# Optimization experiments

Measured on AMD Instinct MI355X. Metric: run time of the kernel, lower is better.

Reference implementation:

```python
import jax, jax.numpy as jnp
import numpy as np

# ControllerLayer hyperparams (match init_kwargs)
ALPHA = 0.01
TOP_K = 2
TEMPERATURE = 1.0  # temperature == 1.0 -> no division (use_temperature False)


def setup_inputs() -> dict:
    key = jax.random.key(0)
    k1, k2 = jax.random.split(key)
    B, H, C, D = 8, 32, 2048, 128  # batch, n_heads(=output_dim), seq_len, head_dim(=input_dim)
    x = jax.random.normal(k1, (B, H, C, D), dtype=jnp.float32)
    # router projection weight, torch nn.Linear(input_dim, output_dim, bias=False) -> W: (output_dim, input_dim)
    W = jax.random.normal(k2, (H, D), dtype=jnp.float32) * (1.0 / np.sqrt(D).astype(np.float32))
    return {"x": x, "W": W}


def reference(x, W):
    # x: (B, H, C, D) -- q reshaped per-head features; W: (O, D) with O == H
    B, H, C, D = x.shape
    O = W.shape[0]
    logits = jnp.einsum('bhcd,od->bhco', x, W)          # router logits
    probs = jax.nn.softmax(logits, axis=-1)             # (B, H, C, O)
    topk_probs, topk_idx = jax.lax.top_k(probs, TOP_K)  # (B, H, C, K)

    # torch.gather along dim=1 (head axis): sel[b,h,c,j,d] = x[b, topk_idx[b,h,c,j], c, d]
    xb = jnp.broadcast_to(x[:, :, :, None, :], (B, H, C, TOP_K, D))
    idx = jnp.broadcast_to(topk_idx[..., None], (B, H, C, TOP_K, D))
    sel = jnp.take_along_axis(xb, idx, axis=1)          # (B, H, C, K, D)

    # weighted sum over the k selected heads
    y = jnp.einsum('bhck,bhckd->bhcd', topk_probs, sel)

    # auxiliary load-balancing loss
    router_probs = probs.mean(axis=(0, 1, 2))                                   # (O,)
    counts = jnp.zeros((O,), jnp.float32).at[topk_idx.ravel()].add(1.0)         # bincount
    router_fraction = counts / counts.sum()
    aux_loss = ALPHA * O * jnp.sum(router_probs * router_fraction)
    return y, aux_loss
```

## Files before the change

kernel.cpp:

```cpp
#include <hip/hip_runtime.h>

#define NSLOT 256

typedef double dbl4 __attribute__((ext_vector_type(4)));
typedef float  f32x4 __attribute__((ext_vector_type(4)));

__global__ __launch_bounds__(256) void convert_w_kernel(const float* __restrict__ W,
                                                        double* __restrict__ wd) {
  int i = blockIdx.x * 256 + threadIdx.x;
  int d4 = i >> 7;
  int o  = (i >> 2) & 31;
  int k  = i & 3;
  wd[i] = (double)W[(o << 7) + (d4 << 2) + k];
}

__global__ __launch_bounds__(256, 4) void moe_router_kernel(
    const float* __restrict__ x, const double* __restrict__ wd,
    float* __restrict__ y, float* __restrict__ ws) {
  __shared__ float  Xs[64 * 128];
  __shared__ double m1s[4][64];
  __shared__ double m2s[4][64];
  __shared__ int    jps[4][64];
  __shared__ float  sumS[4][64];

  const int tid = threadIdx.x;
  const int l   = tid & 63;
  const int wu  = __builtin_amdgcn_readfirstlane(tid >> 6);
  const int bc  = blockIdx.x;
  const int b   = bc >> 10;
  const int c0  = (bc & 1023) << 1;

  const float* xb = x + ((size_t)b * 32 * 2048 + c0) * 128;

  {
    auto ldsX = (__attribute__((address_space(3))) char*)Xs;
    #pragma unroll
    for (int rep = 0; rep < 8; ++rep) {
      int i   = (rep << 8) + tid;
      int row = i >> 5;
      int p   = i & 31;
      int h   = row & 31, t = row >> 5;
      int d4  = p ^ (row & 31);
      const float* src = xb + ((size_t)h * 2048 + t) * 128 + (d4 << 2);
      __builtin_amdgcn_global_load_lds(
          (const __attribute__((address_space(1))) void*)src,
          (__attribute__((address_space(3))) void*)(ldsX + (size_t)i * 16),
          16, 0, 0);
    }
  }
  __syncthreads();

  double acc[8] = {0, 0, 0, 0, 0, 0, 0, 0};
  const dbl4* __restrict__ wv4 = reinterpret_cast<const dbl4*>(wd);
  const int rsw = l & 31;
  #pragma unroll 2
  for (int d4 = 0; d4 < 32; ++d4) {
    float4 xv = *reinterpret_cast<const float4*>(&Xs[(l << 7) + ((d4 ^ rsw) << 2)]);
    double x0 = (double)xv.x, x1 = (double)xv.y, x2 = (double)xv.z, x3 = (double)xv.w;
    const dbl4* wc = wv4 + (d4 << 5) + (wu << 3);
    #pragma unroll
    for (int j = 0; j < 8; ++j) {
      dbl4 wj = wc[j];
      acc[j] = fma(x0, wj[0], acc[j]);
      acc[j] = fma(x1, wj[1], acc[j]);
      acc[j] = fma(x2, wj[2], acc[j]);
      acc[j] = fma(x3, wj[3], acc[j]);
    }
  }

  double m1 = acc[0], m2 = -1.0e300;
  int    j1 = 0, j2 = 0;
  #pragma unroll
  for (int j = 1; j < 8; ++j) {
    double v = acc[j];
    if (v > m1)      { m2 = m1; j2 = j1; m1 = v; j1 = j; }
    else if (v > m2) { m2 = v; j2 = j; }
  }
  float e[8];
  float sloc = 0.0f;
  #pragma unroll
  for (int j = 0; j < 8; ++j) { e[j] = __expf((float)(acc[j] - m1)); sloc += e[j]; }

  m1s[wu][l]  = m1;
  m2s[wu][l]  = m2;
  jps[wu][l]  = (j1 + (wu << 3)) | ((j2 + (wu << 3)) << 8);
  sumS[wu][l] = sloc;
  __syncthreads();

  double M = -1.0e300, g2 = -1.0e300;
  int g1i = 0, g2i = 0;
  #pragma unroll
  for (int w = 0; w < 4; ++w) {
    double a  = m1s[w][l];
    double bb = m2s[w][l];
    int    jp = jps[w][l];
    if (a > M)       { g2 = M; g2i = g1i; M = a; g1i = jp & 255; }
    else if (a > g2) { g2 = a; g2i = jp & 255; }
    if (bb > g2)     { g2 = bb; g2i = (jp >> 8) & 255; }
  }
  float S = 0.0f;
  #pragma unroll
  for (int w = 0; w < 4; ++w)
    S += sumS[w][l] * __expf((float)(m1s[w][l] - M));
  const float invS = 1.0f / S;
  const float p1 = invS;
  const float p2 = __expf((float)(g2 - M)) * invS;
  const int   jpack = g1i | (g2i << 8);

  {
    const float f = __expf((float)(m1 - M)) * invS;
    float ps[8];
    #pragma unroll
    for (int j = 0; j < 8; ++j) ps[j] = e[j] * f;
    #pragma unroll
    for (int m = 1; m < 64; m <<= 1) {
      #pragma unroll
      for (int j = 0; j < 8; ++j) ps[j] += __shfl_xor(ps[j], m, 64);
    }
    const int slot = (bc & (NSLOT - 1)) << 5;
    if (l == 0) {
      #pragma unroll
      for (int j = 0; j < 8; ++j) atomicAdd(&ws[slot + (wu << 3) + j], ps[j]);
    }
    if (wu == 0) {
      float cnt = 0.0f;
      #pragma unroll
      for (int o = 0; o < 32; ++o) {
        float c = (float)(__popcll(__ballot(g1i == o)) + __popcll(__ballot(g2i == o)));
        if (l == o) cnt = c;
      }
      if (l < 32) atomicAdd(&ws[8192 + slot + l], cnt);
    }
  }

  float* yb = y + ((size_t)b * 32 * 2048 + c0) * 128;
  #pragma unroll
  for (int rep = 0; rep < 8; ++rep) {
    int i   = (rep << 8) + tid;
    int row = i >> 5;
    int d4  = i & 31;
    float q1 = __shfl(p1, row, 64);
    float q2 = __shfl(p2, row, 64);
    int   jp = __shfl(jpack, row, 64);
    int i1 = jp & 255, i2 = (jp >> 8) & 255;
    int t = row >> 5, h = row & 31;
    const float4 A  = *reinterpret_cast<const float4*>(
        &Xs[(((t << 5) + i1) << 7) + ((d4 ^ i1) << 2)]);
    const float4 Bv = *reinterpret_cast<const float4*>(
        &Xs[(((t << 5) + i2) << 7) + ((d4 ^ i2) << 2)]);
    f32x4 o4;
    o4.x = q1 * A.x + q2 * Bv.x;
    o4.y = q1 * A.y + q2 * Bv.y;
    o4.z = q1 * A.z + q2 * Bv.z;
    o4.w = q1 * A.w + q2 * Bv.w;
    __builtin_nontemporal_store(o4,
        reinterpret_cast<f32x4*>(yb + ((size_t)h * 2048 + t) * 128 + (d4 << 2)));
  }
}

__global__ __launch_bounds__(256) void finalize_kernel(const float* __restrict__ ws,
                                                       float* __restrict__ out_aux) {
  __shared__ double redP[8][32];
  __shared__ double redC[8][32];
  const int o = threadIdx.x & 31;
  const int g = threadIdx.x >> 5;
  double sp = 0.0, sc = 0.0;
  for (int s = g; s < NSLOT; s += 8) {
    sp += (double)ws[s * 32 + o];
    sc += (double)ws[8192 + s * 32 + o];
  }
  redP[g][o] = sp;
  redC[g][o] = sc;
  __syncthreads();
  if (threadIdx.x == 0) {
    double aux = 0.0;
    const double nrows  = 524288.0;
    const double ntotal = 1048576.0;
    for (int oo = 0; oo < 32; ++oo) {
      double tp = 0.0, tc = 0.0;
      for (int gg = 0; gg < 8; ++gg) { tp += redP[gg][oo]; tc += redC[gg][oo]; }
      aux += (tp / nrows) * (tc / ntotal);
    }
    out_aux[0] = (float)(0.01 * 32.0 * aux);
  }
}

extern "C" void kernel_launch(void* const* d_in, const int* in_sizes, int n_in,
                              void* d_out, int out_size, void* d_ws, size_t ws_size,
                              hipStream_t stream) {
  const float* x = (const float*)d_in[0];
  const float* W = (const float*)d_in[1];
  float*  y  = (float*)d_out;
  float*  ws = (float*)d_ws;
  double* wd = (double*)((char*)d_ws + 65536);

  (void)hipMemsetAsync(d_ws, 0, 16384 * sizeof(float), stream);
  convert_w_kernel<<<16, 256, 0, stream>>>(W, wd);
  moe_router_kernel<<<8192, 256, 0, stream>>>(x, wd, y, ws);
  finalize_kernel<<<1, 256, 0, stream>>>(ws, y + (size_t)8 * 32 * 2048 * 128);
}
```

Before: 194.0 us.

## Use 512-thread blocks splitting experts across 8 waves and fold memset into prep

The router block grows from 4 to 8 wavefronts, so each wave computes logits for 4 experts instead of 8. This halves per-thread FP64 accumulators and adds an LDS prefetch of the next x chunk inside the dot-product loop. The separate hipMemsetAsync is merged into the W-conversion kernel to cut one launch. The cost is a larger cross-wave reduction, more LDS for the per-wave partials, and a different occupancy trade-off.

```diff
diff --git a/kernel.cpp b/kernel.cpp
--- a/kernel.cpp
+++ b/kernel.cpp
@@ -5,23 +5,27 @@
 typedef double dbl4 __attribute__((ext_vector_type(4)));
 typedef float  f32x4 __attribute__((ext_vector_type(4)));
 
-__global__ __launch_bounds__(256) void convert_w_kernel(const float* __restrict__ W,
-                                                        double* __restrict__ wd) {
+__global__ __launch_bounds__(256) void prep_kernel(const float* __restrict__ W,
+                                                   double* __restrict__ wd,
+                                                   float* __restrict__ ws) {
   int i = blockIdx.x * 256 + threadIdx.x;
-  int d4 = i >> 7;
-  int o  = (i >> 2) & 31;
-  int k  = i & 3;
-  wd[i] = (double)W[(o << 7) + (d4 << 2) + k];
-}
-
-__global__ __launch_bounds__(256, 4) void moe_router_kernel(
+  ws[i] = 0.0f;
+  if (i < 4096) {
+    int d4 = i >> 7;
+    int o  = (i >> 2) & 31;
+    int k  = i & 3;
+    wd[i] = (double)W[(o << 7) + (d4 << 2) + k];
+  }
+}
+
+__global__ __launch_bounds__(512, 6) void moe_router_kernel(
     const float* __restrict__ x, const double* __restrict__ wd,
     float* __restrict__ y, float* __restrict__ ws) {
   __shared__ float  Xs[64 * 128];
-  __shared__ double m1s[4][64];
-  __shared__ double m2s[4][64];
-  __shared__ int    jps[4][64];
-  __shared__ float  sumS[4][64];
+  __shared__ double m1s[8][64];
+  __shared__ double m2s[8][64];
+  __shared__ int    jps[8][64];
+  __shared__ float  sumS[8][64];
 
   const int tid = threadIdx.x;
   const int l   = tid & 63;
@@ -35,8 +39,8 @@
   {
     auto ldsX = (__attribute__((address_space(3))) char*)Xs;
     #pragma unroll
-    for (int rep = 0; rep < 8; ++rep) {
-      int i   = (rep << 8) + tid;
+    for (int rep = 0; rep < 4; ++rep) {
+      int i   = (rep << 9) + tid;
       int row = i >> 5;
       int p   = i & 31;
       int h   = row & 31, t = row >> 5;
@@ -50,47 +54,53 @@
   }
   __syncthreads();
 
-  double acc[8] = {0, 0, 0, 0, 0, 0, 0, 0};
+  double a0 = 0.0, a1 = 0.0, a2 = 0.0, a3 = 0.0;
   const dbl4* __restrict__ wv4 = reinterpret_cast<const dbl4*>(wd);
-  const int rsw = l & 31;
-  #pragma unroll 2
+  const int rsw  = l & 31;
+  const int base = l << 7;
+  float4 xv = *reinterpret_cast<const float4*>(&Xs[base + (rsw << 2)]);
+  #pragma unroll 4
   for (int d4 = 0; d4 < 32; ++d4) {
-    float4 xv = *reinterpret_cast<const float4*>(&Xs[(l << 7) + ((d4 ^ rsw) << 2)]);
+    float4 xn = *reinterpret_cast<const float4*>(
+        &Xs[base + ((((d4 + 1) & 31) ^ rsw) << 2)]);
+    const dbl4* wc = wv4 + (d4 << 5) + (wu << 2);
+    dbl4 w0 = wc[0], w1 = wc[1], w2 = wc[2], w3 = wc[3];
     double x0 = (double)xv.x, x1 = (double)xv.y, x2 = (double)xv.z, x3 = (double)xv.w;
-    const dbl4* wc = wv4 + (d4 << 5) + (wu << 3);
-    #pragma unroll
-    for (int j = 0; j < 8; ++j) {
-      dbl4 wj = wc[j];
-      acc[j] = fma(x0, wj[0], acc[j]);
-      acc[j] = fma(x1, wj[1], acc[j]);
-      acc[j] = fma(x2, wj[2], acc[j]);
-      acc[j] = fma(x3, wj[3], acc[j]);
-    }
-  }
-
+    a0 = fma(x0, w0[0], a0); a0 = fma(x1, w0[1], a0);
+    a0 = fma(x2, w0[2], a0); a0 = fma(x3, w0[3], a0);
+    a1 = fma(x0, w1[0], a1); a1 = fma(x1, w1[1], a1);
+    a1 = fma(x2, w1[2], a1); a1 = fma(x3, w1[3], a1);
+    a2 = fma(x0, w2[0], a2); a2 = fma(x1, w2[1], a2);
+    a2 = fma(x2, w2[2], a2); a2 = fma(x3, w2[3], a2);
+    a3 = fma(x0, w3[0], a3); a3 = fma(x1, w3[1], a3);
+    a3 = fma(x2, w3[2], a3); a3 = fma(x3, w3[3], a3);
+    xv = xn;
+  }
+
+  double acc[4] = {a0, a1, a2, a3};
   double m1 = acc[0], m2 = -1.0e300;
   int    j1 = 0, j2 = 0;
   #pragma unroll
-  for (int j = 1; j < 8; ++j) {
+  for (int j = 1; j < 4; ++j) {
     double v = acc[j];
     if (v > m1)      { m2 = m1; j2 = j1; m1 = v; j1 = j; }
     else if (v > m2) { m2 = v; j2 = j; }
   }
-  float e[8];
+  float e[4];
   float sloc = 0.0f;
   #pragma unroll
-  for (int j = 0; j < 8; ++j) { e[j] = __expf((float)(acc[j] - m1)); sloc += e[j]; }
+  for (int j = 0; j < 4; ++j) { e[j] = __expf((float)(acc[j] - m1)); sloc += e[j]; }
 
   m1s[wu][l]  = m1;
   m2s[wu][l]  = m2;
-  jps[wu][l]  = (j1 + (wu << 3)) | ((j2 + (wu << 3)) << 8);
+  jps[wu][l]  = (j1 + (wu << 2)) | ((j2 + (wu << 2)) << 8);
   sumS[wu][l] = sloc;
   __syncthreads();
 
   double M = -1.0e300, g2 = -1.0e300;
   int g1i = 0, g2i = 0;
   #pragma unroll
-  for (int w = 0; w < 4; ++w) {
+  for (int w = 0; w < 8; ++w) {
     double a  = m1s[w][l];
     double bb = m2s[w][l];
     int    jp = jps[w][l];
@@ -100,7 +110,7 @@
   }
   float S = 0.0f;
   #pragma unroll
-  for (int w = 0; w < 4; ++w)
+  for (int w = 0; w < 8; ++w)
     S += sumS[w][l] * __expf((float)(m1s[w][l] - M));
   const float invS = 1.0f / S;
   const float p1 = invS;
@@ -109,18 +119,18 @@
 
   {
     const float f = __expf((float)(m1 - M)) * invS;
-    float ps[8];
+    float ps[4];
     #pragma unroll
-    for (int j = 0; j < 8; ++j) ps[j] = e[j] * f;
+    for (int j = 0; j < 4; ++j) ps[j] = e[j] * f;
     #pragma unroll
     for (int m = 1; m < 64; m <<= 1) {
       #pragma unroll
-      for (int j = 0; j < 8; ++j) ps[j] += __shfl_xor(ps[j], m, 64);
+      for (int j = 0; j < 4; ++j) ps[j] += __shfl_xor(ps[j], m, 64);
     }
     const int slot = (bc & (NSLOT - 1)) << 5;
     if (l == 0) {
       #pragma unroll
-      for (int j = 0; j < 8; ++j) atomicAdd(&ws[slot + (wu << 3) + j], ps[j]);
+      for (int j = 0; j < 4; ++j) atomicAdd(&ws[slot + (wu << 2) + j], ps[j]);
     }
     if (wu == 0) {
       float cnt = 0.0f;
@@ -135,8 +145,8 @@
 
   float* yb = y + ((size_t)b * 32 * 2048 + c0) * 128;
   #pragma unroll
-  for (int rep = 0; rep < 8; ++rep) {
-    int i   = (rep << 8) + tid;
+  for (int rep = 0; rep < 4; ++rep) {
+    int i   = (rep << 9) + tid;
     int row = i >> 5;
     int d4  = i & 31;
     float q1 = __shfl(p1, row, 64);
@@ -194,8 +204,7 @@
   float*  ws = (float*)d_ws;
   double* wd = (double*)((char*)d_ws + 65536);
 
-  (void)hipMemsetAsync(d_ws, 0, 16384 * sizeof(float), stream);
-  convert_w_kernel<<<16, 256, 0, stream>>>(W, wd);
-  moe_router_kernel<<<8192, 256, 0, stream>>>(x, wd, y, ws);
+  prep_kernel<<<64, 256, 0, stream>>>(W, wd, ws);
+  moe_router_kernel<<<8192, 512, 0, stream>>>(x, wd, y, ws);
   finalize_kernel<<<1, 256, 0, stream>>>(ws, y + (size_t)8 * 32 * 2048 * 128);
 }
```

Measured after the change: 175.8 us. -9.4%, faster.
